# Optimization experiments

Hardware: AMD Instinct MI355X
Metric: run time of the kernel (lower is better)

Reference implementation:

```python
import jax, jax.numpy as jnp
import numpy as np

N, E, IN_DIM, OUT_DIM, SEM_DIM = 50000, 800000, 128, 128, 128
EPS = 1e-8


def setup_inputs() -> dict:
    key = jax.random.key(0)
    k = jax.random.split(key, 8)
    x = jax.random.normal(k[0], (N, IN_DIM), dtype=jnp.float32)
    edge_index = jax.random.randint(k[1], (2, E), 0, N, dtype=jnp.int64)
    semantic_vec = jax.random.normal(k[2], (N, SEM_DIM), dtype=jnp.float32)
    s = 1.0 / np.sqrt(IN_DIM)
    W_src = jax.random.uniform(k[3], (OUT_DIM, IN_DIM), jnp.float32, -s, s)
    b_src = jax.random.uniform(k[4], (OUT_DIM,), jnp.float32, -s, s)
    W_dst = jax.random.uniform(k[5], (OUT_DIM, IN_DIM), jnp.float32, -s, s)
    b_dst = jax.random.uniform(k[6], (OUT_DIM,), jnp.float32, -s, s)
    return {"x": x, "edge_index": edge_index, "semantic_vec": semantic_vec,
            "W_src": W_src, "b_src": b_src, "W_dst": W_dst, "b_dst": b_dst}


def _scatter_softmax(sim, dst, num_segments):
    # numerically stable segment-wise softmax over edges grouped by dst
    seg_max = jax.ops.segment_max(sim, dst, num_segments=num_segments)
    seg_max = jnp.where(jnp.isneginf(seg_max), 0.0, seg_max)
    e = jnp.exp(sim - seg_max[dst])
    seg_sum = jax.ops.segment_sum(e, dst, num_segments=num_segments)
    return e / (seg_sum[dst] + 1e-16)


def reference(x, edge_index, semantic_vec, W_src, b_src, W_dst, b_dst):
    src, dst = edge_index[0], edge_index[1]
    x_j = x[src] @ W_src.T + b_src           # [E, out_dim]
    # cosine similarity with torch eps semantics
    a = semantic_vec[src]
    b = semantic_vec[dst]
    na = jnp.maximum(jnp.linalg.norm(a, axis=-1), EPS)
    nb = jnp.maximum(jnp.linalg.norm(b, axis=-1), EPS)
    sim = jnp.sum(a * b, axis=-1) / (na * nb)  # [E]
    attn = _scatter_softmax(sim, dst, x.shape[0])
    msg = attn[:, None] * x_j                 # [E, out_dim]
    out = jax.ops.segment_sum(msg, dst, num_segments=x.shape[0])
    return out
```

## Files before the change

kernel.cpp:

```cpp
#include <hip/hip_runtime.h>
#include <hip/hip_fp16.h>

#define Nn 50000
#define Ee 800000
#define D  128
#define SLOT 64

#define B_SCAT 782
#define B_NORM 3125

struct h4 { __half2 lo, hi; };

typedef _Float16 f16x8 __attribute__((ext_vector_type(8)));
typedef float    f32x4 __attribute__((ext_vector_type(4)));

__global__ __launch_bounds__(256) void k_gemm(const float* __restrict__ x,
                                              const float* __restrict__ W,
                                              const float* __restrict__ b,
                                              __half* __restrict__ y16,
                                              int* __restrict__ cnt) {
  __shared__ __half sW16[128 * 136] __attribute__((aligned(16)));
  __shared__ __half sA16[64 * 136]  __attribute__((aligned(16)));
  int bid = blockIdx.x, tid = threadIdx.x;
  int n0 = bid * 64;

  if (tid < 16) {
    int idx = bid * 64 + tid * 4;
    *(int4*)(cnt + idx) = (int4){0, 0, 0, 0};
  }

  for (int r = 0; r < 16; r++) {
    int i = tid + 256 * r;
    int row = i >> 5, c4 = (i & 31) << 2;
    float4 w = *(const float4*)(W + (size_t)row * 128 + c4);
    __half2* dst = (__half2*)&sW16[row * 136 + c4];
    dst[0] = __floats2half2_rn(w.x, w.y);
    dst[1] = __floats2half2_rn(w.z, w.w);
  }
  for (int r = 0; r < 8; r++) {
    int i = tid + 256 * r;
    int row = i >> 5, c4 = (i & 31) << 2;
    int nr = n0 + row; if (nr >= Nn) nr = Nn - 1;
    float4 v = *(const float4*)(x + (size_t)nr * 128 + c4);
    __half2* dst = (__half2*)&sA16[row * 136 + c4];
    dst[0] = __floats2half2_rn(v.x, v.y);
    dst[1] = __floats2half2_rn(v.z, v.w);
  }
  __syncthreads();

  int wave = tid >> 6, lane = tid & 63;
  int g = lane >> 4, n16 = lane & 15;
  int m0 = n0 + wave * 16;

  f32x4 acc[8];
#pragma unroll
  for (int jt = 0; jt < 8; jt++) {
    float bias = b[jt * 16 + n16];
    acc[jt] = (f32x4){bias, bias, bias, bias};
  }

#pragma unroll
  for (int kt = 0; kt < 4; kt++) {
    f16x8 a = *(const f16x8*)(&sA16[(wave * 16 + n16) * 136 + kt * 32 + g * 8]);
#pragma unroll
    for (int jt = 0; jt < 8; jt++) {
      f16x8 bf = *(const f16x8*)(&sW16[(jt * 16 + n16) * 136 + kt * 32 + g * 8]);
      acc[jt] = __builtin_amdgcn_mfma_f32_16x16x32_f16(a, bf, acc[jt], 0, 0, 0);
    }
  }

#pragma unroll
  for (int jt = 0; jt < 8; jt++) {
#pragma unroll
    for (int r = 0; r < 4; r++) {
      int row = m0 + g * 4 + r;
      if (row < Nn)
        y16[(size_t)row * 128 + jt * 16 + n16] = __float2half(acc[jt][r]);
    }
  }
}

__global__ __launch_bounds__(256) void k_prep2(const int* __restrict__ ei,
                                               const float* __restrict__ sem,
                                               __half* __restrict__ sem16,
                                               int* __restrict__ cnt,
                                               unsigned short* __restrict__ slot16) {
  int bid = blockIdx.x, tid = threadIdx.x;
  if (bid < B_SCAT) {
    int base = bid * 1024 + tid;
#pragma unroll
    for (int u = 0; u < 4; u++) {
      int e = base + u * 256;
      if (e < Ee) {
        int s = ei[e], d = ei[Ee + e];
        int pos = atomicAdd(cnt + d, 1);
        if (pos < SLOT)
          slot16[(size_t)d * SLOT + pos] = (unsigned short)s;
      }
    }
  } else {
    int nb = (bid - B_SCAT) * 16;
    int wave = tid >> 6, lane = tid & 63;
#pragma unroll
    for (int it = 0; it < 4; it++) {
      int n = nb + it * 4 + wave;
      const float2 v = *(const float2*)(sem + (size_t)n * D + 2 * lane);
      float p = v.x * v.x + v.y * v.y;
#pragma unroll
      for (int off = 32; off > 0; off >>= 1) p += __shfl_xor(p, off);
      float inv = 1.0f / fmaxf(sqrtf(p), 1e-8f);
      *(__half2*)(sem16 + (size_t)n * D + 2 * lane) = __floats2half2_rn(v.x * inv, v.y * inv);
    }
  }
}

__global__ __launch_bounds__(256) void k_fused(const __half* __restrict__ sem16,
                                               const __half* __restrict__ y16,
                                               const unsigned short* __restrict__ slot16,
                                               const int* __restrict__ cnt,
                                               float* __restrict__ out) {
  int d = (blockIdx.x * 256 + threadIdx.x) >> 6;
  int lane = threadIdx.x & 63;
  if (d >= Nn) return;
  int sub = lane >> 5, l32 = lane & 31;
  int c = cnt[d]; if (c > SLOT) c = SLOT;

  int sv = (lane < c) ? (int)slot16[(size_t)d * SLOT + lane] : 0;

  h4 dref = ((const h4*)(sem16 + (size_t)d * D))[l32];
  float2 d0 = __half22float2(dref.lo), d1 = __half22float2(dref.hi);

  float Sp = 0.0f;
  float o0 = 0, o1 = 0, o2 = 0, o3 = 0;
  for (int i = 0; i < c; i += 4) {
    int ia = i + sub, ib = i + 2 + sub;
    int ca = ia < c ? ia : c - 1, cb = ib < c ? ib : c - 1;
    int sa = __shfl(sv, ca), sb = __shfl(sv, cb);
    h4 ra = ((const h4*)(sem16 + (size_t)sa * D))[l32];
    h4 rb = ((const h4*)(sem16 + (size_t)sb * D))[l32];
    h4 ya = ((const h4*)(y16 + (size_t)sa * D))[l32];
    h4 yb = ((const h4*)(y16 + (size_t)sb * D))[l32];
    float2 ra0 = __half22float2(ra.lo), ra1 = __half22float2(ra.hi);
    float2 rb0 = __half22float2(rb.lo), rb1 = __half22float2(rb.hi);
    float pa = d0.x * ra0.x + d0.y * ra0.y + d1.x * ra1.x + d1.y * ra1.y;
    float pb = d0.x * rb0.x + d0.y * rb0.y + d1.x * rb1.x + d1.y * rb1.y;
#pragma unroll
    for (int o = 16; o > 0; o >>= 1) { pa += __shfl_xor(pa, o); pb += __shfl_xor(pb, o); }
    float ea = __expf(pa); if (ia >= c) ea = 0.0f;
    float eb = __expf(pb); if (ib >= c) eb = 0.0f;
    Sp += ea + eb;
    float2 a0 = __half22float2(ya.lo), a1 = __half22float2(ya.hi);
    float2 b0 = __half22float2(yb.lo), b1 = __half22float2(yb.hi);
    o0 += ea * a0.x + eb * b0.x;
    o1 += ea * a0.y + eb * b0.y;
    o2 += ea * a1.x + eb * b1.x;
    o3 += ea * a1.y + eb * b1.y;
  }
  Sp += __shfl_xor(Sp, 32);
  o0 += __shfl_xor(o0, 32); o1 += __shfl_xor(o1, 32);
  o2 += __shfl_xor(o2, 32); o3 += __shfl_xor(o3, 32);
  if (sub == 0) {
    float inv = 1.0f / (Sp + 1e-16f);
    float4 r; r.x = o0 * inv; r.y = o1 * inv; r.z = o2 * inv; r.w = o3 * inv;
    *(float4*)(out + (size_t)d * D + l32 * 4) = r;
  }
}

extern "C" void kernel_launch(void* const* d_in, const int* in_sizes, int n_in,
                              void* d_out, int out_size, void* d_ws, size_t ws_size,
                              hipStream_t stream) {
  const float* x     = (const float*)d_in[0];
  const int*   ei    = (const int*)d_in[1];
  const float* sem   = (const float*)d_in[2];
  const float* W_src = (const float*)d_in[3];
  const float* b_src = (const float*)d_in[4];
  float* out = (float*)d_out;

  char* ws = (char*)d_ws;
  const size_t O_Y    = 0;
  const size_t O_S16  = 12800000;
  const size_t O_CNT  = 25600000;
  const size_t O_SS   = 25804800;
  const size_t NEED   = 32204800;
  if (ws_size < NEED) return;

  __half* y16   = (__half*)(ws + O_Y);
  __half* sem16 = (__half*)(ws + O_S16);
  int* cnt = (int*)(ws + O_CNT);
  unsigned short* slot16 = (unsigned short*)(ws + O_SS);

  k_gemm<<<(Nn + 63) / 64, 256, 0, stream>>>(x, W_src, b_src, y16, cnt);
  k_prep2<<<B_SCAT + B_NORM, 256, 0, stream>>>(ei, sem, sem16, cnt, slot16);
  k_fused<<<(Nn + 3) / 4, 256, 0, stream>>>(sem16, y16, slot16, cnt, out);
}
```

Baseline: 206.1 us.

## Interleave normalized semantics and projected features per node, regroup kernels, use fdot2

Packs the normalized fp16 semantic vector and the fp16 projected feature of each node into one 512-byte row. The gather in the fused kernel then touches one contiguous row per neighbor instead of two separate arrays. The semantic normalization moves into the GEMM launch as extra blocks, and the edge scatter becomes its own kernel. The cosine dot product uses the packed fp16 fdot2 builtin. The risks are a different launch grouping (the scatter no longer overlaps with the normalization) and fdot2 precision.

```diff
diff --git a/kernel.cpp b/kernel.cpp
--- a/kernel.cpp
+++ b/kernel.cpp
@@ -5,117 +5,133 @@
 #define Ee 800000
 #define D  128
 #define SLOT 64
-
+#define PKS 256
+
+#define B_GEMM 782
+#define B_NORM 782
 #define B_SCAT 782
-#define B_NORM 3125
 
 struct h4 { __half2 lo, hi; };
 
 typedef _Float16 f16x8 __attribute__((ext_vector_type(8)));
+typedef _Float16 f16x2 __attribute__((ext_vector_type(2)));
 typedef float    f32x4 __attribute__((ext_vector_type(4)));
 
-__global__ __launch_bounds__(256) void k_gemm(const float* __restrict__ x,
-                                              const float* __restrict__ W,
-                                              const float* __restrict__ b,
-                                              __half* __restrict__ y16,
-                                              int* __restrict__ cnt) {
+union H2 { __half2 h; f16x2 v; };
+
+__device__ __forceinline__ float dot4(h4 a, h4 b, float acc) {
+#if __has_builtin(__builtin_amdgcn_fdot2)
+  H2 al, ah, bl, bh;
+  al.h = a.lo; ah.h = a.hi; bl.h = b.lo; bh.h = b.hi;
+  acc = __builtin_amdgcn_fdot2(al.v, bl.v, acc, false);
+  return __builtin_amdgcn_fdot2(ah.v, bh.v, acc, false);
+#else
+  float2 a0 = __half22float2(a.lo), a1 = __half22float2(a.hi);
+  float2 b0 = __half22float2(b.lo), b1 = __half22float2(b.hi);
+  return acc + a0.x * b0.x + a0.y * b0.y + a1.x * b1.x + a1.y * b1.y;
+#endif
+}
+
+__global__ __launch_bounds__(256) void k_gemm_norm(const float* __restrict__ x,
+                                                   const float* __restrict__ W,
+                                                   const float* __restrict__ b,
+                                                   const float* __restrict__ sem,
+                                                   __half* __restrict__ pk,
+                                                   int* __restrict__ cnt) {
   __shared__ __half sW16[128 * 136] __attribute__((aligned(16)));
   __shared__ __half sA16[64 * 136]  __attribute__((aligned(16)));
   int bid = blockIdx.x, tid = threadIdx.x;
-  int n0 = bid * 64;
-
-  if (tid < 16) {
-    int idx = bid * 64 + tid * 4;
-    *(int4*)(cnt + idx) = (int4){0, 0, 0, 0};
-  }
-
-  for (int r = 0; r < 16; r++) {
-    int i = tid + 256 * r;
-    int row = i >> 5, c4 = (i & 31) << 2;
-    float4 w = *(const float4*)(W + (size_t)row * 128 + c4);
-    __half2* dst = (__half2*)&sW16[row * 136 + c4];
-    dst[0] = __floats2half2_rn(w.x, w.y);
-    dst[1] = __floats2half2_rn(w.z, w.w);
-  }
-  for (int r = 0; r < 8; r++) {
-    int i = tid + 256 * r;
-    int row = i >> 5, c4 = (i & 31) << 2;
-    int nr = n0 + row; if (nr >= Nn) nr = Nn - 1;
-    float4 v = *(const float4*)(x + (size_t)nr * 128 + c4);
-    __half2* dst = (__half2*)&sA16[row * 136 + c4];
-    dst[0] = __floats2half2_rn(v.x, v.y);
-    dst[1] = __floats2half2_rn(v.z, v.w);
-  }
-  __syncthreads();
-
-  int wave = tid >> 6, lane = tid & 63;
-  int g = lane >> 4, n16 = lane & 15;
-  int m0 = n0 + wave * 16;
-
-  f32x4 acc[8];
-#pragma unroll
-  for (int jt = 0; jt < 8; jt++) {
-    float bias = b[jt * 16 + n16];
-    acc[jt] = (f32x4){bias, bias, bias, bias};
-  }
-
-#pragma unroll
-  for (int kt = 0; kt < 4; kt++) {
-    f16x8 a = *(const f16x8*)(&sA16[(wave * 16 + n16) * 136 + kt * 32 + g * 8]);
+
+  if (bid < B_GEMM) {
+    int n0 = bid * 64;
+    if (tid < 16) {
+      int idx = n0 + tid * 4;
+      *(int4*)(cnt + idx) = (int4){0, 0, 0, 0};
+    }
+    for (int r = 0; r < 16; r++) {
+      int i = tid + 256 * r;
+      int row = i >> 5, c4 = (i & 31) << 2;
+      float4 w = *(const float4*)(W + (size_t)row * 128 + c4);
+      __half2* dst = (__half2*)&sW16[row * 136 + c4];
+      dst[0] = __floats2half2_rn(w.x, w.y);
+      dst[1] = __floats2half2_rn(w.z, w.w);
+    }
+    for (int r = 0; r < 8; r++) {
+      int i = tid + 256 * r;
+      int row = i >> 5, c4 = (i & 31) << 2;
+      int nr = n0 + row; if (nr >= Nn) nr = Nn - 1;
+      float4 v = *(const float4*)(x + (size_t)nr * 128 + c4);
+      __half2* dst = (__half2*)&sA16[row * 136 + c4];
+      dst[0] = __floats2half2_rn(v.x, v.y);
+      dst[1] = __floats2half2_rn(v.z, v.w);
+    }
+    __syncthreads();
+
+    int wave = tid >> 6, lane = tid & 63;
+    int g = lane >> 4, n16 = lane & 15;
+    int m0 = n0 + wave * 16;
+
+    f32x4 acc[8];
 #pragma unroll
     for (int jt = 0; jt < 8; jt++) {
-      f16x8 bf = *(const f16x8*)(&sW16[(jt * 16 + n16) * 136 + kt * 32 + g * 8]);
-      acc[jt] = __builtin_amdgcn_mfma_f32_16x16x32_f16(a, bf, acc[jt], 0, 0, 0);
-    }
-  }
-
-#pragma unroll
-  for (int jt = 0; jt < 8; jt++) {
-#pragma unroll
-    for (int r = 0; r < 4; r++) {
-      int row = m0 + g * 4 + r;
-      if (row < Nn)
-        y16[(size_t)row * 128 + jt * 16 + n16] = __float2half(acc[jt][r]);
-    }
-  }
-}
-
-__global__ __launch_bounds__(256) void k_prep2(const int* __restrict__ ei,
-                                               const float* __restrict__ sem,
-                                               __half* __restrict__ sem16,
-                                               int* __restrict__ cnt,
-                                               unsigned short* __restrict__ slot16) {
-  int bid = blockIdx.x, tid = threadIdx.x;
-  if (bid < B_SCAT) {
-    int base = bid * 1024 + tid;
-#pragma unroll
-    for (int u = 0; u < 4; u++) {
-      int e = base + u * 256;
-      if (e < Ee) {
-        int s = ei[e], d = ei[Ee + e];
-        int pos = atomicAdd(cnt + d, 1);
-        if (pos < SLOT)
-          slot16[(size_t)d * SLOT + pos] = (unsigned short)s;
+      float bias = b[jt * 16 + n16];
+      acc[jt] = (f32x4){bias, bias, bias, bias};
+    }
+
+#pragma unroll
+    for (int kt = 0; kt < 4; kt++) {
+      f16x8 a = *(const f16x8*)(&sA16[(wave * 16 + n16) * 136 + kt * 32 + g * 8]);
+#pragma unroll
+      for (int jt = 0; jt < 8; jt++) {
+        f16x8 bf = *(const f16x8*)(&sW16[(jt * 16 + n16) * 136 + kt * 32 + g * 8]);
+        acc[jt] = __builtin_amdgcn_mfma_f32_16x16x32_f16(a, bf, acc[jt], 0, 0, 0);
       }
     }
+
+#pragma unroll
+    for (int jt = 0; jt < 8; jt++) {
+#pragma unroll
+      for (int r = 0; r < 4; r++) {
+        int row = m0 + g * 4 + r;
+        if (row < Nn)
+          pk[(size_t)row * PKS + 128 + jt * 16 + n16] = __float2half(acc[jt][r]);
+      }
+    }
   } else {
-    int nb = (bid - B_SCAT) * 16;
+    int nb = (bid - B_GEMM) * 64;
     int wave = tid >> 6, lane = tid & 63;
 #pragma unroll
-    for (int it = 0; it < 4; it++) {
-      int n = nb + it * 4 + wave;
-      const float2 v = *(const float2*)(sem + (size_t)n * D + 2 * lane);
-      float p = v.x * v.x + v.y * v.y;
-#pragma unroll
-      for (int off = 32; off > 0; off >>= 1) p += __shfl_xor(p, off);
-      float inv = 1.0f / fmaxf(sqrtf(p), 1e-8f);
-      *(__half2*)(sem16 + (size_t)n * D + 2 * lane) = __floats2half2_rn(v.x * inv, v.y * inv);
-    }
-  }
-}
-
-__global__ __launch_bounds__(256) void k_fused(const __half* __restrict__ sem16,
-                                               const __half* __restrict__ y16,
+    for (int it = 0; it < 16; it++) {
+      int n = nb + wave * 16 + it;
+      if (n < Nn) {
+        const float2 v = *(const float2*)(sem + (size_t)n * D + 2 * lane);
+        float p = v.x * v.x + v.y * v.y;
+#pragma unroll
+        for (int off = 32; off > 0; off >>= 1) p += __shfl_xor(p, off);
+        float inv = 1.0f / fmaxf(sqrtf(p), 1e-8f);
+        *(__half2*)(pk + (size_t)n * PKS + 2 * lane) = __floats2half2_rn(v.x * inv, v.y * inv);
+      }
+    }
+  }
+}
+
+__global__ __launch_bounds__(256) void k_scat(const int* __restrict__ ei,
+                                              int* __restrict__ cnt,
+                                              unsigned short* __restrict__ slot16) {
+  int base = blockIdx.x * 1024 + threadIdx.x;
+#pragma unroll
+  for (int u = 0; u < 4; u++) {
+    int e = base + u * 256;
+    if (e < Ee) {
+      int s = ei[e], d = ei[Ee + e];
+      int pos = atomicAdd(cnt + d, 1);
+      if (pos < SLOT)
+        slot16[(size_t)d * SLOT + pos] = (unsigned short)s;
+    }
+  }
+}
+
+__global__ __launch_bounds__(256) void k_fused(const __half* __restrict__ pk,
                                                const unsigned short* __restrict__ slot16,
                                                const int* __restrict__ cnt,
                                                float* __restrict__ out) {
@@ -127,8 +143,7 @@
 
   int sv = (lane < c) ? (int)slot16[(size_t)d * SLOT + lane] : 0;
 
-  h4 dref = ((const h4*)(sem16 + (size_t)d * D))[l32];
-  float2 d0 = __half22float2(dref.lo), d1 = __half22float2(dref.hi);
+  h4 dref = ((const h4*)(pk + (size_t)d * PKS))[l32];
 
   float Sp = 0.0f;
   float o0 = 0, o1 = 0, o2 = 0, o3 = 0;
@@ -136,14 +151,14 @@
     int ia = i + sub, ib = i + 2 + sub;
     int ca = ia < c ? ia : c - 1, cb = ib < c ? ib : c - 1;
     int sa = __shfl(sv, ca), sb = __shfl(sv, cb);
-    h4 ra = ((const h4*)(sem16 + (size_t)sa * D))[l32];
-    h4 rb = ((const h4*)(sem16 + (size_t)sb * D))[l32];
-    h4 ya = ((const h4*)(y16 + (size_t)sa * D))[l32];
-    h4 yb = ((const h4*)(y16 + (size_t)sb * D))[l32];
-    float2 ra0 = __half22float2(ra.lo), ra1 = __half22float2(ra.hi);
-    float2 rb0 = __half22float2(rb.lo), rb1 = __half22float2(rb.hi);
-    float pa = d0.x * ra0.x + d0.y * ra0.y + d1.x * ra1.x + d1.y * ra1.y;
-    float pb = d0.x * rb0.x + d0.y * rb0.y + d1.x * rb1.x + d1.y * rb1.y;
+    const __half* pa_ = pk + (size_t)sa * PKS;
+    const __half* pb_ = pk + (size_t)sb * PKS;
+    h4 ra = ((const h4*)pa_)[l32];
+    h4 ya = ((const h4*)(pa_ + 128))[l32];
+    h4 rb = ((const h4*)pb_)[l32];
+    h4 yb = ((const h4*)(pb_ + 128))[l32];
+    float pa = dot4(dref, ra, 0.0f);
+    float pb = dot4(dref, rb, 0.0f);
 #pragma unroll
     for (int o = 16; o > 0; o >>= 1) { pa += __shfl_xor(pa, o); pb += __shfl_xor(pb, o); }
     float ea = __expf(pa); if (ia >= c) ea = 0.0f;
@@ -177,19 +192,17 @@
   float* out = (float*)d_out;
 
   char* ws = (char*)d_ws;
-  const size_t O_Y    = 0;
-  const size_t O_S16  = 12800000;
+  const size_t O_PK   = 0;
   const size_t O_CNT  = 25600000;
   const size_t O_SS   = 25804800;
   const size_t NEED   = 32204800;
   if (ws_size < NEED) return;
 
-  __half* y16   = (__half*)(ws + O_Y);
-  __half* sem16 = (__half*)(ws + O_S16);
+  __half* pk = (__half*)(ws + O_PK);
   int* cnt = (int*)(ws + O_CNT);
   unsigned short* slot16 = (unsigned short*)(ws + O_SS);
 
-  k_gemm<<<(Nn + 63) / 64, 256, 0, stream>>>(x, W_src, b_src, y16, cnt);
-  k_prep2<<<B_SCAT + B_NORM, 256, 0, stream>>>(ei, sem, sem16, cnt, slot16);
-  k_fused<<<(Nn + 3) / 4, 256, 0, stream>>>(sem16, y16, slot16, cnt, out);
-}
+  k_gemm_norm<<<B_GEMM + B_NORM, 256, 0, stream>>>(x, W_src, b_src, sem, pk, cnt);
+  k_scat<<<B_SCAT, 256, 0, stream>>>(ei, cnt, slot16);
+  k_fused<<<(Nn + 3) / 4, 256, 0, stream>>>(pk, slot16, cnt, out);
+}
```

Result: slower. 232.8 us (+13.0%).
